# Optimization experiments

Measured on AMD Instinct MI355X. Metric: run time of the kernel, lower is better.

## Reference

```python
import jax, jax.numpy as jnp
import numpy as np

SR = 44100
LOWEST = 82.0
L_ORDER = 5
NUM_COEFF = L_ORDER + 1          # 6
NUM_ACTIVE = NUM_COEFF + 1       # 7 (linear interp)
K = int(SR // LOWEST) + NUM_ACTIVE  # coeff_vector_size = 544
N_FRAMES = 100
EXC_FRAMES = 100
EXC_ORDER = 5
BURST_LEN = 2048
N_SAMPLES = 44100


def upsample_linear(frames, T):
    """Linear interpolation of (F,) or (F, C) control frames to T samples (align_corners)."""
    F_ = frames.shape[0]
    pos = jnp.linspace(0.0, F_ - 1.0, T)
    i0 = jnp.clip(jnp.floor(pos).astype(jnp.int32), 0, F_ - 2)
    w = pos - i0.astype(pos.dtype)
    lo = frames[i0]
    hi = frames[i0 + 1]
    if frames.ndim == 2:
        w = w[:, None]
    return lo + (hi - lo) * w


def sample_wise_lpc(x, A):
    """Time-varying all-pole filter: y[t] = x[t] - sum_k A[t,k] * y[t-k-1].
    x: (T,), A: (T, N) -> y: (T,)"""
    N = A.shape[1]

    def step(buf, inp):
        xt, at = inp
        y = xt - jnp.dot(at, buf)  # buf[0]=y[t-1], ..., buf[N-1]=y[t-N]
        buf = jnp.concatenate([y[None], buf[:-1]])
        return buf, y

    _, y = jax.lax.scan(step, jnp.zeros((N,), x.dtype), (x, A))
    return y


def _forward(delay_len_frames, excitation, raw_coeff_frames, raw_gain, exc_coefficients, n_samples):
    T = n_samples
    # --- upsample control signals to audio rate ---
    delay = upsample_linear(delay_len_frames, T)                     # (T,)
    gain = jax.nn.sigmoid(raw_gain) * 0.1 + 0.9
    sb = jax.nn.sigmoid(raw_coeff_frames)                            # (F, 6)
    coeff_frames = sb / sb.sum(axis=-1, keepdims=True) * gain        # normalized, stable
    b = upsample_linear(coeff_frames, T)                             # (T, 6)

    # --- build sparse banded A (linear fractional-delay interpolation) ---
    z_l = jnp.floor(delay).astype(jnp.int32)                         # integer delay
    alfa = delay - z_l.astype(delay.dtype)                           # fractional part
    v0 = -(1.0 - alfa) * b[:, 0]                                     # (T,)
    vmid = -(alfa[:, None] * b[:, :-1] + (1.0 - alfa)[:, None] * b[:, 1:])  # (T, 5)
    vlast = -alfa * b[:, -1]                                         # (T,)
    vals = jnp.concatenate([v0[:, None], vmid, vlast[:, None]], axis=1)     # (T, 7)
    idxs = z_l[:, None] + jnp.arange(NUM_ACTIVE)[None, :]            # (T, 7)
    A = jnp.zeros((T, K), delay.dtype).at[jnp.arange(T)[:, None], idxs].set(vals)

    # --- excitation shaping filter (requires_grad branch) ---
    burst = excitation                                               # (BURST_LEN,)
    a_exc = upsample_linear(exc_coefficients, burst.shape[0])        # (BURST_LEN, 5)
    filtered_burst = sample_wise_lpc(burst, a_exc)

    # --- Karplus-Strong loop: time-varying all-pole with banded A ---
    x = jnp.zeros((T,), burst.dtype).at[: burst.shape[0]].set(filtered_burst)
    y = sample_wise_lpc(x, A)
    return y.astype(jnp.float32)


def setup_inputs() -> dict:
    key = jax.random.key(0)
    k0, k1, k2, k3 = jax.random.split(key, 4)
    # delay in [100, 520] samples so floor(delay)+NUM_ACTIVE-1 < K = 544
    delay_len_frames = 100.0 + 420.0 * jax.random.uniform(k0, (N_FRAMES,), dtype=jnp.float32)
    excitation = jax.random.normal(k1, (BURST_LEN,), dtype=jnp.float32)
    raw_coeff_frames = jax.random.uniform(k2, (N_FRAMES, NUM_COEFF), dtype=jnp.float32,
                                          minval=-2.0, maxval=0.0)
    raw_gain = jnp.asarray(0.0, dtype=jnp.float32)
    exc_coefficients = 0.01 * jax.random.normal(k3, (EXC_FRAMES, EXC_ORDER), dtype=jnp.float32)
    return {
        "delay_len_frames": delay_len_frames,
        "excitation": excitation,
        "raw_coeff_frames": raw_coeff_frames,
        "raw_gain": raw_gain,
        "exc_coefficients": exc_coefficients,
        "n_samples": N_SAMPLES,
    }


def reference(delay_len_frames, excitation, raw_coeff_frames, raw_gain, exc_coefficients, n_samples):
    return _forward(delay_len_frames, excitation, raw_coeff_frames, raw_gain,
                    exc_coefficients, n_samples)
```

## Files before the change

kernel.cpp:

```cpp
#include <hip/hip_runtime.h>
#include <math.h>


#define T_SAMPLES 44100
#define NFRAMES   100
#define NCOEF     6
#define BURST     2048
#define EXC_ORD   5

#define HISTSZ    1096
#define GRPF      9600
#define CFBUF     9856

#define WS_COEF_FLOATS (T_SAMPLES * 12)
#define WS_EXC_OFF     WS_COEF_FLOATS
#define WS_EXC_FLOATS  (EXC_ORD * BURST)
#define WS_TOTAL_BYTES ((size_t)(WS_COEF_FLOATS + WS_EXC_FLOATS) * 4)

__global__ __launch_bounds__(256) void diffks_precompute(
    const float* __restrict__ delay_frames,
    const float* __restrict__ raw_coeff,
    const float* __restrict__ raw_gain,
    const float* __restrict__ exc_coeff,
    float* __restrict__ ws)
{
    int g = blockIdx.x * 256 + threadIdx.x;
    const float gain = 0.1f / (1.0f + expf(-raw_gain[0])) + 0.9f;

    if (g < T_SAMPLES) {
        const float stepT = 99.0f / (float)(T_SAMPLES - 1);
        float pos = (float)g * stepT;
        int i0 = (int)pos; if (i0 > NFRAMES - 2) i0 = NFRAMES - 2;
        float w = pos - (float)i0;

        float d0 = delay_frames[i0], d1 = delay_frames[i0 + 1];
        float delay = d0 + (d1 - d0) * w;
        int z = (int)delay;
        float alfa = delay - (float)z;

        float b[NCOEF];
        {
            float c0v[NCOEF], c1v[NCOEF];
            float s0 = 0.f, s1 = 0.f;
            #pragma unroll
            for (int j = 0; j < NCOEF; ++j) {
                c0v[j] = 1.0f / (1.0f + expf(-raw_coeff[i0 * NCOEF + j]));
                c1v[j] = 1.0f / (1.0f + expf(-raw_coeff[(i0 + 1) * NCOEF + j]));
                s0 += c0v[j]; s1 += c1v[j];
            }
            float g0 = gain / s0, g1 = gain / s1;
            #pragma unroll
            for (int j = 0; j < NCOEF; ++j) {
                float x0 = c0v[j] * g0, x1 = c1v[j] * g1;
                b[j] = x0 + (x1 - x0) * w;
            }
        }
        float oma = 1.0f - alfa;
        float v0 = -oma * b[0];
        float v1 = -(alfa * b[0] + oma * b[1]);
        float v2 = -(alfa * b[1] + oma * b[2]);
        float v3 = -(alfa * b[2] + oma * b[3]);
        float v4 = -(alfa * b[3] + oma * b[4]);
        float v5 = -(alfa * b[4] + oma * b[5]);
        float v6 = -alfa * b[5];
        float pv0 = -v0, pv1 = -v1, pv2 = -v2, pv3 = -v3;
        float pv4 = -v4, pv5 = -v5, pv6 = -v6;

        int base = g - z - 1;
        int q = base - 6;
        int off = q & 1;
        unsigned b2 = ((unsigned)q) & 1022u;

        float m0, m1, m2, m3, m4, m5, m6, m7;
        if (off) { m0 = 0.f; m1 = pv6; m2 = pv5; m3 = pv4;
                   m4 = pv3; m5 = pv2; m6 = pv1; m7 = pv0; }
        else     { m0 = pv6; m1 = pv5; m2 = pv4; m3 = pv3;
                   m4 = pv2; m5 = pv1; m6 = pv0; m7 = 0.f; }

        float4* o = (float4*)(ws + (size_t)g * 12);
        o[0] = make_float4(m0, m1, m2, m3);
        o[1] = make_float4(m4, m5, m6, m7);
        o[2] = make_float4(__int_as_float((int)b2), 0.f, 0.f, 0.f);
    } else if (g < T_SAMPLES + BURST) {
        int te = g - T_SAMPLES;
        const float stepE = 99.0f / (float)(BURST - 1);
        float pos = (float)te * stepE;
        int i0 = (int)pos; if (i0 > NFRAMES - 2) i0 = NFRAMES - 2;
        float w = pos - (float)i0;
        float* o = ws + WS_EXC_OFF + te * EXC_ORD;
        #pragma unroll
        for (int k = 0; k < EXC_ORD; ++k) {
            float a0 = exc_coeff[i0 * EXC_ORD + k];
            float a1 = exc_coeff[(i0 + 1) * EXC_ORD + k];
            o[k] = a0 + (a1 - a0) * w;
        }
    }
}

__device__ __forceinline__ void gload_lds16(const float* g, float* l) {
    __builtin_amdgcn_global_load_lds(
        (const __attribute__((address_space(1))) unsigned int*)(g),
        (__attribute__((address_space(3))) unsigned int*)(l),
        16, 0, 0);
}

__global__ __launch_bounds__(256, 1) void diffks_serial(
    const float* __restrict__ excitation,
    const float* __restrict__ ws,
    float* __restrict__ out)
{
    __shared__ float s_cf[2][CFBUF];
    __shared__ float s_x[64][33];
    __shared__ float s_a[64][161];
    __shared__ float s_hist[HISTSZ];
    __shared__ float s_tail[64][32];
    __shared__ float s_bound[64][6];

    const int tid  = threadIdx.x;
    const int lane = tid & 63;
    const int wv   = tid >> 6;

    for (int t = tid; t < BURST; t += 256)
        s_x[t >> 5][t & 31] = excitation[t];
    for (int i = 0; i < 8; ++i) {
        int t = tid + i * 256;
        const float* g = ws + WS_EXC_OFF + t * EXC_ORD;
        float* dst = &s_a[t >> 5][(t & 31) * 5];
        dst[0] = g[0]; dst[1] = g[1]; dst[2] = g[2];
        dst[3] = g[3]; dst[4] = g[4];
    }
    for (int i = tid; i < HISTSZ; i += 256) s_hist[i] = 0.0f;
    __syncthreads();

    if (tid < 64) {
        float st[6][5];
        #pragma unroll
        for (int r = 0; r < 6; ++r)
            #pragma unroll
            for (int k = 0; k < 5; ++k) st[r][k] = 0.0f;
        #pragma unroll
        for (int r = 1; r <= 5; ++r) st[r][r - 1] = 1.0f;

        const float* ar = &s_a[lane][0];
        const float* xr = &s_x[lane][0];
        #pragma unroll 8
        for (int i = 0; i < 32; ++i) {
            float a0 = ar[i * 5 + 0], a1 = ar[i * 5 + 1], a2 = ar[i * 5 + 2];
            float a3 = ar[i * 5 + 3], a4 = ar[i * 5 + 4];
            float xv = xr[i];
            #pragma unroll
            for (int r = 0; r < 6; ++r) {
                float acc = (r == 0) ? xv : 0.0f;
                acc = fmaf(-a0, st[r][0], acc);
                acc = fmaf(-a1, st[r][1], acc);
                acc = fmaf(-a2, st[r][2], acc);
                acc = fmaf(-a3, st[r][3], acc);
                acc = fmaf(-a4, st[r][4], acc);
                st[r][4] = st[r][3]; st[r][3] = st[r][2];
                st[r][2] = st[r][1]; st[r][1] = st[r][0];
                st[r][0] = acc;
            }
        }
        #pragma unroll
        for (int r = 0; r < 6; ++r)
            #pragma unroll
            for (int k = 0; k < 5; ++k)
                s_tail[lane][r * 5 + k] = st[r][k];
    }
    __syncthreads();

    if (tid == 0) {
        float Y[5] = {0.f, 0.f, 0.f, 0.f, 0.f};
        for (int l = 0; l < 64; ++l) {
            #pragma unroll
            for (int c = 0; c < 5; ++c) s_bound[l][c] = Y[c];
            float tl[30];
            #pragma unroll
            for (int j = 0; j < 30; ++j) tl[j] = s_tail[l][j];
            float ny[5];
            #pragma unroll
            for (int k = 0; k < 5; ++k) {
                float acc = tl[k];
                #pragma unroll
                for (int c = 1; c <= 5; ++c)
                    acc = fmaf(tl[c * 5 + k], Y[c - 1], acc);
                ny[k] = acc;
            }
            #pragma unroll
            for (int k = 0; k < 5; ++k) Y[k] = ny[k];
        }
    }
    __syncthreads();

    if (tid < 64) {
        float b0 = s_bound[lane][0], b1 = s_bound[lane][1], b2 = s_bound[lane][2];
        float b3 = s_bound[lane][3], b4 = s_bound[lane][4];
        const float* ar = &s_a[lane][0];
        float* xr = &s_x[lane][0];
        #pragma unroll 8
        for (int i = 0; i < 32; ++i) {
            float a0 = ar[i * 5 + 0], a1 = ar[i * 5 + 1], a2 = ar[i * 5 + 2];
            float a3 = ar[i * 5 + 3], a4 = ar[i * 5 + 4];
            float acc = xr[i];
            acc = fmaf(-a0, b0, acc);
            acc = fmaf(-a1, b1, acc);
            acc = fmaf(-a2, b2, acc);
            acc = fmaf(-a3, b3, acc);
            acc = fmaf(-a4, b4, acc);
            b4 = b3; b3 = b2; b2 = b1; b1 = b0; b0 = acc;
            xr[i] = acc;
        }
    }
    __syncthreads();

    const bool lane_act = (lane < 50);
    const unsigned dumpA = 1032u + (unsigned)lane;

    #define STAGE_GRP(gg)                                                      \
    {                                                                          \
        float* dstb = &s_cf[(gg) & 1][0];                                      \
        const float* srcb = ws + (size_t)(gg) * GRPF + lane * 4;               \
        const int nis = ((gg) >= 55) ? 5 : 38;                                 \
        for (int i = 0; i < nis; ++i)                                          \
            gload_lds16(srcb + i * 256, dstb + i * 256);                       \
    }

    float4 p0a0, p0a1, p0b0, p0b1, p1a0, p1a1, p1b0, p1b1;
    float4 p2a0, p2a1, p2b0, p2b1, p3a0, p3a1, p3b0, p3b1;
    unsigned q0A, q0B, q1A, q1B, q2A, q2B, q3A, q3B;
    unsigned w0A, w0B, w1A, w1B, w2A, w2B, w3A, w3B;
    unsigned m0A, m0B, m1A, m1B, m2A, m2B, m3A, m3B;
    float x0A, x0B, x1A, x1B, x2A, x2B, x3A, x3B;

    #define PREPJ(J, BB)                                                       \
    {                                                                          \
        int b_ = (BB); if (b_ > 440) b_ = 440;                                 \
        const float* bu_ = &s_cf[(b_ >> 3) & 1][0];                            \
        const int ln_ = (b_ & 7) * 100 + lane;                                 \
        const float4* qA_ = (const float4*)(bu_ + ln_ * 12);                   \
        const float4* qB_ = (const float4*)(bu_ + (ln_ + 50) * 12);            \
        p##J##a0 = qA_[0]; p##J##a1 = qA_[1];                                  \
        q##J##A = (unsigned)__float_as_int(qA_[2].x);                          \
        p##J##b0 = qB_[0]; p##J##b1 = qB_[1];                                  \
        q##J##B = (unsigned)__float_as_int(qB_[2].x);                          \
        const int tA_ = b_ * 100 + lane;                                       \
        const int tB_ = tA_ + 50;                                              \
        x##J##A = (lane_act && tA_ < BURST)                                    \
                      ? s_x[(tA_ >> 5) & 63][tA_ & 31] : 0.0f;                 \
        x##J##B = (lane_act && tB_ < BURST)                                    \
                      ? s_x[(tB_ >> 5) & 63][tB_ & 31] : 0.0f;                 \
        const unsigned pA_ = ((unsigned)tA_) & 1023u;                          \
        const unsigned pB_ = ((unsigned)tB_) & 1023u;                          \
        w##J##A = lane_act ? pA_ : dumpA;                                      \
        w##J##B = lane_act ? pB_ : dumpA;                                      \
        m##J##A = (lane_act && pA_ < 6u) ? (pA_ + 1024u) : dumpA;              \
        m##J##B = (lane_act && pB_ < 6u) ? (pB_ + 1024u) : dumpA;              \
    }

    #define PREP4(SS)                                                          \
    {                                                                          \
        const int sb_ = (SS) * 4;                                              \
        PREPJ(0, sb_ + 0) PREPJ(1, sb_ + 1)                                    \
        PREPJ(2, sb_ + 2) PREPJ(3, sb_ + 3)                                    \
    }

    #define CBODY(J)                                                           \
    {                                                                          \
        const float2* wA_ = (const float2*)(s_hist + q##J##A);                 \
        const float2* wB_ = (const float2*)(s_hist + q##J##B);                 \
        const float2 a01_ = wA_[0], a23_ = wA_[1];                             \
        const float2 a45_ = wA_[2], a67_ = wA_[3];                             \
        const float2 b01_ = wB_[0], b23_ = wB_[1];                             \
        const float2 b45_ = wB_[2], b67_ = wB_[3];                             \
        float accA = x##J##A, accB = x##J##B;                                  \
        accA = fmaf(p##J##a1.w, a67_.y, accA);                                 \
        accB = fmaf(p##J##b1.w, b67_.y, accB);                                 \
        accA = fmaf(p##J##a1.z, a67_.x, accA);                                 \
        accB = fmaf(p##J##b1.z, b67_.x, accB);                                 \
        accA = fmaf(p##J##a1.y, a45_.y, accA);                                 \
        accB = fmaf(p##J##b1.y, b45_.y, accB);                                 \
        accA = fmaf(p##J##a1.x, a45_.x, accA);                                 \
        accB = fmaf(p##J##b1.x, b45_.x, accB);                                 \
        accA = fmaf(p##J##a0.w, a23_.y, accA);                                 \
        accB = fmaf(p##J##b0.w, b23_.y, accB);                                 \
        accA = fmaf(p##J##a0.z, a23_.x, accA);                                 \
        accB = fmaf(p##J##b0.z, b23_.x, accB);                                 \
        accA = fmaf(p##J##a0.y, a01_.y, accA);                                 \
        accB = fmaf(p##J##b0.y, b01_.y, accB);                                 \
        accA = fmaf(p##J##a0.x, a01_.x, accA);                                 \
        accB = fmaf(p##J##b0.x, b01_.x, accB);                                 \
        s_hist[w##J##A] = accA;                                                \
        s_hist[w##J##B] = accB;                                                \
        s_hist[m##J##A] = accA;                                                \
        s_hist[m##J##B] = accB;                                                \
    }

    #define COMPUTE4() { CBODY(0) CBODY(1) CBODY(2) CBODY(3) }

    if (wv == 1) {
        STAGE_GRP(0)
        asm volatile("s_waitcnt vmcnt(0)" ::: "memory");
    }
    __syncthreads();
    if (wv == 0) { PREP4(0) }
    __syncthreads();

    #pragma unroll 1
    for (int ss = 0; ss < 110; ++ss) {
        if (wv == (ss & 3)) { COMPUTE4() }
        if (((ss & 1) == 0) && (ss <= 108) && (wv == ((ss + 2) & 3))) {
            STAGE_GRP((ss >> 1) + 1)
        }
        if ((ss >= 1) && (wv == ((ss + 3) & 3))) {
            const int t0_ = (ss - 1) * 400;
            #pragma unroll
            for (int i = 0; i < 6; ++i) {
                int t_ = t0_ + i * 64 + lane;
                out[t_] = s_hist[((unsigned)t_) & 1023u];
            }
            {
                int t_ = t0_ + 384 + lane;
                if (lane < 16) out[t_] = s_hist[((unsigned)t_) & 1023u];
            }
        }
        if (wv == ((ss + 1) & 3)) {
            asm volatile("s_waitcnt vmcnt(0)" ::: "memory");
            PREP4(ss + 1)
        }
        asm volatile("s_waitcnt lgkmcnt(0)\n\ts_barrier" ::: "memory");
    }
    if (wv == 2) { CBODY(0) }
    asm volatile("s_waitcnt lgkmcnt(0)\n\ts_barrier" ::: "memory");
    {
        int t_ = 43600 + tid;
        out[t_] = s_hist[((unsigned)t_) & 1023u];
        t_ += 256;
        if (t_ < T_SAMPLES) out[t_] = s_hist[((unsigned)t_) & 1023u];
    }

    #undef COMPUTE4
    #undef CBODY
    #undef PREP4
    #undef PREPJ
    #undef STAGE_GRP
}

#define CHUNK_FB  101
#define NCH_FB    ((T_SAMPLES + CHUNK_FB - 1) / CHUNK_FB)
#define HIST_FB   1024

__global__ __launch_bounds__(128) void diffks_fallback(
    const float* __restrict__ delay_frames,
    const float* __restrict__ excitation,
    const float* __restrict__ raw_coeff,
    const float* __restrict__ raw_gain,
    const float* __restrict__ exc_coeff,
    float* __restrict__ out)
{
    __shared__ float s_a[EXC_ORD][BURST];
    __shared__ float s_x[BURST];
    __shared__ float s_hist[HIST_FB];
    __shared__ __align__(16) float s_coef[NFRAMES][8];
    __shared__ float s_delay[NFRAMES];

    const int tid = threadIdx.x;
    const float gain = 0.1f / (1.0f + expf(-raw_gain[0])) + 0.9f;

    for (int i = tid; i < NFRAMES; i += 128) s_delay[i] = delay_frames[i];
    for (int f = tid; f < NFRAMES; f += 128) {
        float sb[NCOEF]; float s = 0.0f;
        #pragma unroll
        for (int j = 0; j < NCOEF; ++j) {
            sb[j] = 1.0f / (1.0f + expf(-raw_coeff[f * NCOEF + j]));
            s += sb[j];
        }
        float inv = gain / s;
        #pragma unroll
        for (int j = 0; j < NCOEF; ++j) s_coef[f][j] = sb[j] * inv;
        s_coef[f][6] = 0.0f; s_coef[f][7] = 0.0f;
    }
    const float stepE = 99.0f / 2047.0f;
    for (int t = tid; t < BURST; t += 128) {
        float pos = (float)t * stepE;
        int i0 = (int)pos; if (i0 > NFRAMES - 2) i0 = NFRAMES - 2;
        float w = pos - (float)i0;
        const float* c0 = exc_coeff + i0 * EXC_ORD;
        #pragma unroll
        for (int k = 0; k < EXC_ORD; ++k) {
            float a0 = c0[k], a1 = c0[k + EXC_ORD];
            s_a[k][t] = a0 + (a1 - a0) * w;
        }
        s_x[t] = excitation[t];
    }
    for (int i = tid; i < HIST_FB; i += 128) s_hist[i] = 0.0f;
    __syncthreads();

    if (tid == 0) {
        float y1 = 0.f, y2 = 0.f, y3 = 0.f, y4 = 0.f, y5 = 0.f;
        #pragma unroll 4
        for (int t = 0; t < BURST; ++t) {
            float p = s_x[t];
            p = fmaf(-s_a[1][t], y2, p);
            p = fmaf(-s_a[2][t], y3, p);
            p = fmaf(-s_a[3][t], y4, p);
            p = fmaf(-s_a[4][t], y5, p);
            float y = fmaf(-s_a[0][t], y1, p);
            s_x[t] = y;
            y5 = y4; y4 = y3; y3 = y2; y2 = y1; y1 = y;
        }
    }
    __syncthreads();

    const float stepT = 99.0f / (float)(T_SAMPLES - 1);
    for (int c = 0; c < NCH_FB; ++c) {
        int t = c * CHUNK_FB + tid;
        if (tid < CHUNK_FB && t < T_SAMPLES) {
            float pos = (float)t * stepT;
            int i0 = (int)pos; if (i0 > NFRAMES - 2) i0 = NFRAMES - 2;
            float w = pos - (float)i0;
            float d0 = s_delay[i0], d1 = s_delay[i0 + 1];
            float delay = d0 + (d1 - d0) * w;
            int z = (int)delay;
            float alfa = delay - (float)z;
            const float4* f0 = reinterpret_cast<const float4*>(s_coef[i0]);
            const float4* f1 = reinterpret_cast<const float4*>(s_coef[i0 + 1]);
            float4 c0a = f0[0], c0b = f0[1];
            float4 c1a = f1[0], c1b = f1[1];
            float b[NCOEF];
            b[0] = c0a.x + (c1a.x - c0a.x) * w;
            b[1] = c0a.y + (c1a.y - c0a.y) * w;
            b[2] = c0a.z + (c1a.z - c0a.z) * w;
            b[3] = c0a.w + (c1a.w - c0a.w) * w;
            b[4] = c0b.x + (c1b.x - c0b.x) * w;
            b[5] = c0b.y + (c1b.y - c0b.y) * w;
            float oma = 1.0f - alfa;
            float v[7];
            v[0] = -oma * b[0];
            #pragma unroll
            for (int j = 1; j <= 5; ++j) v[j] = -(alfa * b[j - 1] + oma * b[j]);
            v[6] = -alfa * b[5];
            float x = (t < BURST) ? s_x[t] : 0.0f;
            int base = t - z - 1;
            float sum = 0.0f;
            #pragma unroll
            for (int j = 0; j < 7; ++j) {
                int idx = base - j;
                float yv = s_hist[idx & (HIST_FB - 1)];
                if (idx < 0) yv = 0.0f;
                sum = fmaf(v[j], yv, sum);
            }
            float y = x - sum;
            s_hist[t & (HIST_FB - 1)] = y;
            out[t] = y;
        }
        __syncthreads();
    }
}

extern "C" void kernel_launch(void* const* d_in, const int* in_sizes, int n_in,
                              void* d_out, int out_size, void* d_ws, size_t ws_size,
                              hipStream_t stream) {
    const float* delay_frames = (const float*)d_in[0];
    const float* excitation   = (const float*)d_in[1];
    const float* raw_coeff    = (const float*)d_in[2];
    const float* raw_gain     = (const float*)d_in[3];
    const float* exc_coeff    = (const float*)d_in[4];
    float* out = (float*)d_out;

    if (ws_size >= WS_TOTAL_BYTES) {
        float* ws = (float*)d_ws;
        int gridA = (T_SAMPLES + BURST + 255) / 256;
        diffks_precompute<<<gridA, 256, 0, stream>>>(delay_frames, raw_coeff,
                                                     raw_gain, exc_coeff, ws);
        diffks_serial<<<1, 256, 0, stream>>>(excitation, ws, out);
    } else {
        diffks_fallback<<<1, 128, 0, stream>>>(delay_frames, excitation,
                                               raw_coeff, raw_gain, exc_coeff, out);
    }
}
```

Baseline: 158.2 us.

## Process eight blocks per serial step with triple-buffered LDS coefficient staging

Doubles the number of 100-sample blocks each wave computes per barrier step from four to eight, halving the barrier-synchronised loop iterations. To support this, the history ring grows to 2048 entries, coefficient staging becomes a triple buffer carved from a shared pool aliased with the startup scratch arrays, and loads for the next blocks are interleaved with compute. Excitation reads are skipped after the burst region. This trades fewer barriers and wave handoffs for a longer serial critical path per wave and higher LDS use.

```diff
diff --git a/kernel.cpp b/kernel.cpp
--- a/kernel.cpp
+++ b/kernel.cpp
@@ -8,9 +8,10 @@
 #define BURST     2048
 #define EXC_ORD   5
 
-#define HISTSZ    1096
+#define HISTSZ    2120
 #define GRPF      9600
 #define CFBUF     9856
+#define POOLF     32448
 
 #define WS_COEF_FLOATS (T_SAMPLES * 12)
 #define WS_EXC_OFF     WS_COEF_FLOATS
@@ -69,7 +70,7 @@
         int base = g - z - 1;
         int q = base - 6;
         int off = q & 1;
-        unsigned b2 = ((unsigned)q) & 1022u;
+        unsigned b2 = ((unsigned)q) & 2046u;
 
         float m0, m1, m2, m3, m4, m5, m6, m7;
         if (off) { m0 = 0.f; m1 = pv6; m2 = pv5; m3 = pv4;
@@ -109,12 +110,13 @@
     const float* __restrict__ ws,
     float* __restrict__ out)
 {
-    __shared__ float s_cf[2][CFBUF];
+    __shared__ float s_pool[POOLF];
     __shared__ float s_x[64][33];
-    __shared__ float s_a[64][161];
     __shared__ float s_hist[HISTSZ];
-    __shared__ float s_tail[64][32];
-    __shared__ float s_bound[64][6];
+
+    float (* const s_a)[161]   = (float(*)[161])(s_pool + 19712);
+    float (* const s_tail)[32] = (float(*)[32])(s_pool + 30016);
+    float (* const s_bound)[6] = (float(*)[6])(s_pool + 32064);
 
     const int tid  = threadIdx.x;
     const int lane = tid & 63;
@@ -214,11 +216,11 @@
     __syncthreads();
 
     const bool lane_act = (lane < 50);
-    const unsigned dumpA = 1032u + (unsigned)lane;
+    const unsigned dumpA = 2056u + (unsigned)lane;
 
     #define STAGE_GRP(gg)                                                      \
     {                                                                          \
-        float* dstb = &s_cf[(gg) & 1][0];                                      \
+        float* dstb = s_pool + ((unsigned)(gg) % 3u) * CFBUF;                  \
         const float* srcb = ws + (size_t)(gg) * GRPF + lane * 4;               \
         const int nis = ((gg) >= 55) ? 5 : 38;                                 \
         for (int i = 0; i < nis; ++i)                                          \
@@ -232,10 +234,10 @@
     unsigned m0A, m0B, m1A, m1B, m2A, m2B, m3A, m3B;
     float x0A, x0B, x1A, x1B, x2A, x2B, x3A, x3B;
 
-    #define PREPJ(J, BB)                                                       \
+    #define PREPJ(J, BB, WXF)                                                  \
     {                                                                          \
         int b_ = (BB); if (b_ > 440) b_ = 440;                                 \
-        const float* bu_ = &s_cf[(b_ >> 3) & 1][0];                            \
+        const float* bu_ = s_pool + ((unsigned)(b_ >> 3) % 3u) * CFBUF;        \
         const int ln_ = (b_ & 7) * 100 + lane;                                 \
         const float4* qA_ = (const float4*)(bu_ + ln_ * 12);                   \
         const float4* qB_ = (const float4*)(bu_ + (ln_ + 50) * 12);            \
@@ -245,23 +247,18 @@
         q##J##B = (unsigned)__float_as_int(qB_[2].x);                          \
         const int tA_ = b_ * 100 + lane;                                       \
         const int tB_ = tA_ + 50;                                              \
-        x##J##A = (lane_act && tA_ < BURST)                                    \
-                      ? s_x[(tA_ >> 5) & 63][tA_ & 31] : 0.0f;                 \
-        x##J##B = (lane_act && tB_ < BURST)                                    \
-                      ? s_x[(tB_ >> 5) & 63][tB_ & 31] : 0.0f;                 \
-        const unsigned pA_ = ((unsigned)tA_) & 1023u;                          \
-        const unsigned pB_ = ((unsigned)tB_) & 1023u;                          \
+        if (WXF) {                                                             \
+            x##J##A = (lane_act && tA_ < BURST)                                \
+                          ? s_x[(tA_ >> 5) & 63][tA_ & 31] : 0.0f;             \
+            x##J##B = (lane_act && tB_ < BURST)                                \
+                          ? s_x[(tB_ >> 5) & 63][tB_ & 31] : 0.0f;             \
+        } else { x##J##A = 0.0f; x##J##B = 0.0f; }                             \
+        const unsigned pA_ = ((unsigned)tA_) & 2047u;                          \
+        const unsigned pB_ = ((unsigned)tB_) & 2047u;                          \
         w##J##A = lane_act ? pA_ : dumpA;                                      \
         w##J##B = lane_act ? pB_ : dumpA;                                      \
-        m##J##A = (lane_act && pA_ < 6u) ? (pA_ + 1024u) : dumpA;              \
-        m##J##B = (lane_act && pB_ < 6u) ? (pB_ + 1024u) : dumpA;              \
-    }
-
-    #define PREP4(SS)                                                          \
-    {                                                                          \
-        const int sb_ = (SS) * 4;                                              \
-        PREPJ(0, sb_ + 0) PREPJ(1, sb_ + 1)                                    \
-        PREPJ(2, sb_ + 2) PREPJ(3, sb_ + 3)                                    \
+        m##J##A = (lane_act && pA_ < 6u) ? (pA_ + 2048u) : dumpA;              \
+        m##J##B = (lane_act && pB_ < 6u) ? (pB_ + 2048u) : dumpA;              \
     }
 
     #define CBODY(J)                                                           \
@@ -295,52 +292,60 @@
         s_hist[m##J##B] = accB;                                                \
     }
 
-    #define COMPUTE4() { CBODY(0) CBODY(1) CBODY(2) CBODY(3) }
-
-    if (wv == 1) {
+    #define STEPBODY(WXF)                                                      \
+    {                                                                          \
+        if (wv == (ss & 3)) {                                                  \
+            const int sb_ = ss * 8;                                            \
+            CBODY(0) PREPJ(0, sb_ + 4, WXF)                                    \
+            CBODY(1) PREPJ(1, sb_ + 5, WXF)                                    \
+            CBODY(2) PREPJ(2, sb_ + 6, WXF)                                    \
+            CBODY(3) PREPJ(3, sb_ + 7, WXF)                                    \
+            CBODY(0) CBODY(1) CBODY(2) CBODY(3)                                \
+        }                                                                      \
+        if ((ss <= 53) && (wv == ((ss + 2) & 3))) { STAGE_GRP(ss + 2) }        \
+        if ((ss >= 1) && (wv == ((ss + 3) & 3))) {                             \
+            const int t0_ = (ss - 1) * 800;                                    \
+            _Pragma("unroll")                                                  \
+            for (int i_ = 0; i_ < 12; ++i_) {                                  \
+                int t_ = t0_ + i_ * 64 + lane;                                 \
+                out[t_] = s_hist[((unsigned)t_) & 2047u];                      \
+            }                                                                  \
+            { int t_ = t0_ + 768 + lane;                                       \
+              if (lane < 32) out[t_] = s_hist[((unsigned)t_) & 2047u]; }       \
+        }                                                                      \
+        if (wv == ((ss + 1) & 3)) {                                            \
+            asm volatile("s_waitcnt vmcnt(0)" ::: "memory");                   \
+            const int nb_ = (ss + 1) * 8;                                      \
+            PREPJ(0, nb_ + 0, WXF) PREPJ(1, nb_ + 1, WXF)                      \
+            PREPJ(2, nb_ + 2, WXF) PREPJ(3, nb_ + 3, WXF)                      \
+        }                                                                      \
+        asm volatile("s_waitcnt lgkmcnt(0)\n\ts_barrier" ::: "memory");        \
+    }
+
+    if (wv == 0) {
         STAGE_GRP(0)
         asm volatile("s_waitcnt vmcnt(0)" ::: "memory");
     }
-    __syncthreads();
-    if (wv == 0) { PREP4(0) }
+    if (wv == 1) { STAGE_GRP(1) }
+    __syncthreads();
+    if (wv == 0) {
+        PREPJ(0, 0, true) PREPJ(1, 1, true)
+        PREPJ(2, 2, true) PREPJ(3, 3, true)
+    }
     __syncthreads();
 
     #pragma unroll 1
-    for (int ss = 0; ss < 110; ++ss) {
-        if (wv == (ss & 3)) { COMPUTE4() }
-        if (((ss & 1) == 0) && (ss <= 108) && (wv == ((ss + 2) & 3))) {
-            STAGE_GRP((ss >> 1) + 1)
-        }
-        if ((ss >= 1) && (wv == ((ss + 3) & 3))) {
-            const int t0_ = (ss - 1) * 400;
-            #pragma unroll
-            for (int i = 0; i < 6; ++i) {
-                int t_ = t0_ + i * 64 + lane;
-                out[t_] = s_hist[((unsigned)t_) & 1023u];
-            }
-            {
-                int t_ = t0_ + 384 + lane;
-                if (lane < 16) out[t_] = s_hist[((unsigned)t_) & 1023u];
-            }
-        }
-        if (wv == ((ss + 1) & 3)) {
-            asm volatile("s_waitcnt vmcnt(0)" ::: "memory");
-            PREP4(ss + 1)
-        }
-        asm volatile("s_waitcnt lgkmcnt(0)\n\ts_barrier" ::: "memory");
-    }
-    if (wv == 2) { CBODY(0) }
+    for (int ss = 0; ss < 3; ++ss) STEPBODY(true)
+    #pragma unroll 1
+    for (int ss = 3; ss < 55; ++ss) STEPBODY(false)
+
+    if (wv == 3) { CBODY(0) }
     asm volatile("s_waitcnt lgkmcnt(0)\n\ts_barrier" ::: "memory");
-    {
-        int t_ = 43600 + tid;
-        out[t_] = s_hist[((unsigned)t_) & 1023u];
-        t_ += 256;
-        if (t_ < T_SAMPLES) out[t_] = s_hist[((unsigned)t_) & 1023u];
-    }
-
-    #undef COMPUTE4
+    for (int t_ = 43200 + tid; t_ < T_SAMPLES; t_ += 256)
+        out[t_] = s_hist[((unsigned)t_) & 2047u];
+
+    #undef STEPBODY
     #undef CBODY
-    #undef PREP4
     #undef PREPJ
     #undef STAGE_GRP
 }
```

New measurement: 154.9 us. 2.1% less time.
